# Kernel optimization log

Hardware: AMD Instinct MI355X
Metric: run time of the kernel (lower is better)

Reference implementation:

```python
import jax, jax.numpy as jnp
import numpy as np
from jax import lax

B, N, F_IN, F_OUT = 64, 256, 768, 256


def setup_inputs() -> dict:
    key = jax.random.key(0)
    ks = jax.random.split(key, 14)
    s = 0.02
    h = jax.random.normal(ks[0], (B, N, F_IN), jnp.float32)
    adj = jax.random.randint(ks[1], (B, N, N), 0, 2).astype(jnp.float32)
    return {
        'h': h,
        'adj': adj,
        'emb_W': jax.random.normal(ks[2], (F_OUT, F_IN), jnp.float32) * s,
        'ioux_W': jax.random.normal(ks[3], (2 * F_OUT, F_OUT), jnp.float32) * s,
        'ioux_b': jax.random.normal(ks[4], (2 * F_OUT,), jnp.float32) * s,
        'iouh_W': jax.random.normal(ks[5], (2 * F_OUT, F_OUT), jnp.float32) * s,
        'iouh_b': jax.random.normal(ks[6], (2 * F_OUT,), jnp.float32) * s,
        'coux_W': jax.random.normal(ks[7], (F_OUT, F_OUT), jnp.float32) * s,
        'coux_b': jax.random.normal(ks[8], (F_OUT,), jnp.float32) * s,
        'couh_W': jax.random.normal(ks[9], (F_OUT, F_OUT), jnp.float32) * s,
        'couh_b': jax.random.normal(ks[10], (F_OUT,), jnp.float32) * s,
        'fc_W': jax.random.normal(ks[11], (2, F_OUT), jnp.float32) * s,
        'fc_b': jax.random.normal(ks[12], (2,), jnp.float32) * s,
    }


def reference(h, adj, emb_W, ioux_W, ioux_b, iouh_W, iouh_b,
              coux_W, coux_b, couh_W, couh_b, fc_W, fc_b):
    # h: [B,N,F_IN], adj: [B,N,N]
    h_e = jnp.einsum('bnf,of->bno', h, emb_W)            # emb(h), no bias
    d = jnp.sum(adj, axis=-1)                            # row-degree [B,N]
    d_inv = jnp.where(d != 0, 1.0 / jnp.where(d != 0, d, 1.0), 0.0)
    # x-side projections depend only on the original h_e -> precompute once
    iou_x = jnp.einsum('bnf,of->bno', h_e, ioux_W) + ioux_b   # [B,N,2F]
    cou_x = jnp.einsum('bnf,of->bno', h_e, coux_W) + coux_b   # [B,N,F]

    n_nodes = h.shape[1]

    def step(h_copy, i):
        # Tree_Parent_AGG row i: p[b,i] = d_inv[b,i] * sum_j adj[b,j,i] * h_copy[b,j]
        adj_col = lax.dynamic_index_in_dim(adj, i, axis=2, keepdims=False)   # [B,N]
        dinv_i = lax.dynamic_index_in_dim(d_inv, i, axis=1, keepdims=False)  # [B]
        x_parent = jnp.einsum('bn,bnd->bd', adj_col, h_copy) * dinv_i[:, None]
        iou = lax.dynamic_index_in_dim(iou_x, i, axis=1, keepdims=False) \
              + x_parent @ iouh_W.T + iouh_b
        r, z = jnp.split(iou, 2, axis=1)
        r = jax.nn.sigmoid(r)
        z = jax.nn.sigmoid(z)
        hc = jnp.tanh(lax.dynamic_index_in_dim(cou_x, i, axis=1, keepdims=False)
                      + (r * x_parent) @ couh_W.T + couh_b)
        h_new = z * x_parent + (1.0 - z) * hc
        h_copy = lax.dynamic_update_index_in_dim(h_copy, h_new, i, axis=1)
        return h_copy, None

    h_final, _ = lax.scan(step, h_e, jnp.arange(n_nodes))
    pooled = jnp.max(h_final, axis=1)                    # [B,F]
    return pooled @ fc_W.T + fc_b                        # [B,2]
```

## Files before the change

kernel.cpp:

```cpp
#include <hip/hip_runtime.h>
#include <hip/hip_fp16.h>

#define NB    64
#define NN    256
#define FIN   768
#define FOUT  256

typedef _Float16 half8v __attribute__((ext_vector_type(8)));
typedef float    float4v __attribute__((ext_vector_type(4)));

__device__ inline unsigned char enc8(float v){
#if __has_builtin(__builtin_amdgcn_cvt_pk_fp8_f32)
  return (unsigned char)(__builtin_amdgcn_cvt_pk_fp8_f32(v, v, 0, false) & 0xFF);
#else
  float best = 1e30f; unsigned char bc = 0;
  for (int c = 0; c < 256; c++){
    if ((c & 0x7F) == 0x7F) continue;
    int e = (c >> 3) & 15, mnt = c & 7;
    float mag = e ? ldexpf(1.f + mnt*0.125f, e-7) : ldexpf(mnt*0.125f, -6);
    float d = (c >> 7) ? -mag : mag;
    float err = fabsf(v - d);
    if (err < best){ best = err; bc = (unsigned char)c; }
  }
  return bc;
#endif
}

__device__ inline float4v mfma_fp8(long long a, long long b, float4v c){
  return __builtin_amdgcn_mfma_f32_16x16x32_fp8_fp8(a, b, c, 0, 0, 0);
}
__device__ inline float4v mfma_f16(half8v a, half8v b, float4v c){
  return __builtin_amdgcn_mfma_f32_16x16x32_f16(a, b, c, 0, 0, 0);
}

__global__ __launch_bounds__(256) void setup_kernel(
    const float* __restrict__ emb_W, const float* __restrict__ ioux_W,
    const float* __restrict__ ioux_b, const float* __restrict__ coux_W,
    const float* __restrict__ coux_b,
    const float* __restrict__ iouh_W, const float* __restrict__ couh_W,
    const float* __restrict__ adj,
    _Float16* __restrict__ embW16, _Float16* __restrict__ Wcat16,
    float* __restrict__ biascat,
    unsigned char* __restrict__ iouh8, unsigned char* __restrict__ couh8,
    float* __restrict__ invrs_iou, float* __restrict__ invrs_cou,
    unsigned int* __restrict__ maskw, float* __restrict__ dinv)
{
  __shared__ float sm[256];
  __shared__ unsigned int rb[256][8];
  const int bid = blockIdx.x;
  const int t   = threadIdx.x;

  if (bid < 1539){
    int idx = bid*256 + t;
    if (idx < 196608) { embW16[idx] = (_Float16)emb_W[idx]; return; }
    idx -= 196608;
    if (idx < 196608) {
      int o = idx >> 8, k = idx & 255;
      float v = (o < 512) ? ioux_W[o*256 + k] : coux_W[(o-512)*256 + k];
      Wcat16[idx] = (_Float16)v; return;
    }
    idx -= 196608;
    if (idx < 768) biascat[idx] = (idx < 512) ? ioux_b[idx] : coux_b[idx-512];
    return;
  }

  if (bid < 2307){
    const int row = bid - 1539;
    const bool is_iou = (row < 512);
    const int rl = is_iou ? row : row - 512;
    const float w = is_iou ? iouh_W[(size_t)rl*256 + t] : couh_W[(size_t)rl*256 + t];
    sm[t] = fabsf(w);
    __syncthreads();
    for (int s = 128; s > 0; s >>= 1){
      if (t < s) sm[t] = fmaxf(sm[t], sm[t+s]);
      __syncthreads();
    }
    const float mx = sm[0];
    const float rs = (mx > 1e-20f) ? (240.0f / mx) : 1.0f;
    const unsigned char byte = enc8(w * rs);
    const int off = ((rl>>4)*8 + (t>>5))*512 + ((t>>3)&3)*128 + (rl&15)*8 + (t&7);
    if (is_iou) iouh8[off] = byte; else couh8[off] = byte;
    if (t == 0){
      const float inv = 1.0f / (rs * 16.0f);
      if (is_iou) invrs_iou[rl] = inv; else invrs_cou[rl] = inv;
    }
    return;
  }

  {
    const int b = bid - 2307;
    const float* rowp = adj + (size_t)b*NN*NN + (size_t)t*NN;
    float s = 0.f;
    #pragma unroll
    for (int qc = 0; qc < 8; qc++){
      unsigned int w = 0;
      const float4* rp = (const float4*)(rowp + qc*32);
      #pragma unroll
      for (int j4 = 0; j4 < 8; j4++){
        float4 v = rp[j4];
        s += v.x + v.y + v.z + v.w;
        const int sh = j4*4;
        w |= (v.x != 0.f ? 1u : 0u) << sh;
        w |= (v.y != 0.f ? 1u : 0u) << (sh+1);
        w |= (v.z != 0.f ? 1u : 0u) << (sh+2);
        w |= (v.w != 0.f ? 1u : 0u) << (sh+3);
      }
      rb[t][qc] = w;
    }
    dinv[b*NN + t] = (s != 0.f) ? 1.0f/s : 0.0f;
    __syncthreads();
    #pragma unroll
    for (int qc = 0; qc < 8; qc++){
      unsigned int w = 0;
      #pragma unroll
      for (int jj = 0; jj < 32; jj++)
        w |= ((rb[qc*32 + jj][t>>5] >> (t&31)) & 1u) << jj;
      maskw[((size_t)b*NN + t)*8 + qc] = w;
    }
  }
}

template<int AF32, int NTL>
__global__ __launch_bounds__(256) void gemm16_kernel(
    const void* __restrict__ Aq, const _Float16* __restrict__ Bw,
    _Float16* __restrict__ Cout, const float* __restrict__ bias,
    int M, int N, int K, int ldc)
{
  const int wave = threadIdx.x >> 6;
  const int lane = threadIdx.x & 63;
  const int m0 = (blockIdx.x*4 + wave)*16;
  const int n0 = blockIdx.y*(16*NTL);
  const int mrow = m0 + (lane & 15);
  const int kgrp = lane >> 4;
  float4v acc[NTL];
  #pragma unroll
  for (int nt = 0; nt < NTL; nt++) acc[nt] = (float4v){0.f,0.f,0.f,0.f};

  for (int k0 = 0; k0 < K; k0 += 32){
    const int ka = k0 + kgrp*8;
    half8v af;
    if (AF32){
      const float* A = (const float*)Aq;
      const float4* ap = (const float4*)(A + (size_t)mrow*K + ka);
      float4 a0 = ap[0], a1 = ap[1];
      af[0]=(_Float16)a0.x; af[1]=(_Float16)a0.y; af[2]=(_Float16)a0.z; af[3]=(_Float16)a0.w;
      af[4]=(_Float16)a1.x; af[5]=(_Float16)a1.y; af[6]=(_Float16)a1.z; af[7]=(_Float16)a1.w;
    } else {
      const _Float16* A = (const _Float16*)Aq;
      af = *(const half8v*)(A + (size_t)mrow*K + ka);
    }
    #pragma unroll
    for (int nt = 0; nt < NTL; nt++){
      const int ncol = n0 + nt*16 + (lane & 15);
      half8v bf = *(const half8v*)(Bw + (size_t)ncol*K + ka);
      acc[nt] = __builtin_amdgcn_mfma_f32_16x16x32_f16(af, bf, acc[nt], 0, 0, 0);
    }
  }
  #pragma unroll
  for (int nt = 0; nt < NTL; nt++){
    const int ncol = n0 + nt*16 + (lane & 15);
    const float bv = bias ? bias[ncol] : 0.f;
    #pragma unroll
    for (int r = 0; r < 4; r++){
      const int orow = m0 + (lane>>4)*4 + r;
      Cout[(size_t)orow*ldc + ncol] = (_Float16)(acc[nt][r] + bv);
    }
  }
}

__global__ __launch_bounds__(256) void tail_kernel(
    const _Float16* __restrict__ Hc, const _Float16* __restrict__ Wcat16,
    const float* __restrict__ biascat,
    _Float16* __restrict__ OUTX, _Float16* __restrict__ HcT)
{
  __shared__ _Float16 tile[32][264];
  const int bid = blockIdx.x;
  const int t   = threadIdx.x;

  if (bid < 1536){
    const int bx = bid & 255, seg = bid >> 8;
    const int wave = t >> 6;
    const int lane = t & 63;
    const int m0 = (bx*4 + wave)*16;
    const int n0 = seg*128;
    const int mrow = m0 + (lane & 15);
    const int kgrp = lane >> 4;
    float4v acc[8];
    #pragma unroll
    for (int nt = 0; nt < 8; nt++) acc[nt] = (float4v){0.f,0.f,0.f,0.f};
    for (int k0 = 0; k0 < 256; k0 += 32){
      const int ka = k0 + kgrp*8;
      const half8v af = *(const half8v*)(Hc + (size_t)mrow*256 + ka);
      #pragma unroll
      for (int nt = 0; nt < 8; nt++){
        const int ncol = n0 + nt*16 + (lane & 15);
        half8v bf = *(const half8v*)(Wcat16 + (size_t)ncol*256 + ka);
        acc[nt] = __builtin_amdgcn_mfma_f32_16x16x32_f16(af, bf, acc[nt], 0, 0, 0);
      }
    }
    #pragma unroll
    for (int nt = 0; nt < 8; nt++){
      const int ncol = n0 + nt*16 + (lane & 15);
      const float bv = biascat[ncol];
      #pragma unroll
      for (int r = 0; r < 4; r++){
        const int orow = m0 + (lane>>4)*4 + r;
        OUTX[(size_t)orow*768 + ncol] = (_Float16)(acc[nt][r] + bv);
      }
    }
    return;
  }

  {
    const int idx = bid - 1536;
    const int b = idx & 63, fg = idx >> 6;
    #pragma unroll
    for (int pass = 0; pass < 4; pass++){
      const int n  = pass*64 + (t>>2);
      const int f8 = (t&3)*8;
      const half8v v = *(const half8v*)(Hc + (size_t)(b*NN + n)*FOUT + fg*32 + f8);
      #pragma unroll
      for (int e = 0; e < 8; e++) tile[f8+e][n] = v[e];
    }
    __syncthreads();
    const int f = t>>3, ch = t&7;
    _Float16* dst = HcT + ((size_t)b*FOUT + fg*32 + f)*NN + ch*32;
    #pragma unroll
    for (int k = 0; k < 4; k++)
      *(half8v*)(dst + k*8) = *(const half8v*)(&tile[f][ch*32 + k*8]);
  }
}

#define OFF_BT   0
#define OFF_DT   33280
#define OFF_HNT  53760
#define OFF_XP32 74240
#define OFF_XP8  75264
#define OFF_P8   75520
#define OFF_Z    75776
#define OFF_PM   76800
#define OFF_MASK 77824
#define OFF_DINV 86016
#define SCAN_LDS 87040

__global__ __launch_bounds__(512, 2)
void scan_kernel(
    const _Float16* __restrict__ Hc,
    const _Float16* __restrict__ HcT,
    const _Float16* __restrict__ OUTX,
    const unsigned char* __restrict__ iouh8,
    const unsigned char* __restrict__ couh8,
    const float* __restrict__ invrs_iou,
    const float* __restrict__ invrs_cou,
    const float* __restrict__ dinv,
    const unsigned int* __restrict__ maskw,
    const float* __restrict__ iouh_b,
    const float* __restrict__ couh_b,
    const float* __restrict__ fc_W,
    const float* __restrict__ fc_b,
    float* __restrict__ out)
{
  const int b    = blockIdx.x;
  const int t    = threadIdx.x;
  const int wave = t >> 6;
  const int lane = t & 63;
  const int q    = lane >> 4;
  const int r    = lane & 15;
  const int f0   = 32*wave;

  extern __shared__ __align__(16) char smem[];
  float*         sh_xp32 = (float*)(smem + OFF_XP32);
  unsigned char* sh_xp8  = (unsigned char*)(smem + OFF_XP8);
  unsigned char* sh_p8   = (unsigned char*)(smem + OFF_P8);
  float*         sh_z    = (float*)(smem + OFF_Z);
  float*         sh_pm   = (float*)(smem + OFF_PM);
  unsigned int*  sh_mask = (unsigned int*)(smem + OFF_MASK);
  float*         sh_dinv = (float*)(smem + OFF_DINV);

  #pragma unroll
  for (int k = 0; k < 10; k++)
    ((unsigned int*)(smem + OFF_DT))[k*512 + t] = 0u;
  {
    const unsigned int* mg = maskw + ((size_t)b*NN)*8;
    #pragma unroll
    for (int k = 0; k < 4; k++) sh_mask[k*512 + t] = mg[k*512 + t];
    if (t < 256) sh_dinv[t] = dinv[(size_t)b*NN + t];
  }

  half8v Hreg[2][8];
  #pragma unroll
  for (int g = 0; g < 2; g++){
    const _Float16* hp = HcT + ((size_t)b*FOUT + f0 + 16*g + r)*NN + q*8;
    #pragma unroll
    for (int ks = 0; ks < 8; ks++)
      Hreg[g][ks] = *(const half8v*)(hp + ks*32);
  }

  long long ifrag[4][8];
  #pragma unroll
  for (int tt = 0; tt < 4; tt++)
    #pragma unroll
    for (int kc = 0; kc < 8; kc++)
      ifrag[tt][kc] = *(const long long*)(iouh8 + (size_t)(((4*wave+tt)*8 + kc)*512) + q*128 + r*8);
  long long cfrag[2][8];
  #pragma unroll
  for (int tt = 0; tt < 2; tt++)
    #pragma unroll
    for (int kc = 0; kc < 8; kc++)
      cfrag[tt][kc] = *(const long long*)(couh8 + (size_t)(((2*wave+tt)*8 + kc)*512) + q*128 + r*8);

  const int o1    = 64*wave + 16*(r>>2) + q*4 + (r&3);
  const int o_upd = 32*wave + 16*((r>>2)&1) + q*4 + (r&3);
  const float bi1 = iouh_b[o1];
  const float vi1 = invrs_iou[o1];
  const float bcou_l = couh_b[o_upd];
  const float invc_l = invrs_cou[o_upd];
  float pmax = -1e30f;

  __syncthreads();
  unsigned int wl_cur = sh_mask[0];

  #pragma unroll 1
  for (int i = 0; i < NN; i++){
    const size_t row = (size_t)b*NN + i;

    if ((i & 31) == 0){
      const int tile = i >> 5;
      if (tile > 0){
        const int tprev = tile - 1;
        #pragma unroll
        for (int g = 0; g < 2; g++){
          const half8v hv = *(const half8v*)(smem + OFF_HNT + (f0 + 16*g + r)*80 + q*16);
          #pragma unroll
          for (int ks = 0; ks < 8; ks++) if (ks == tprev) Hreg[g][ks] = hv;
        }
      }
      float4v bacc[2][2];
      #pragma unroll
      for (int rt = 0; rt < 2; rt++)
        #pragma unroll
        for (int g = 0; g < 2; g++) bacc[rt][g] = (float4v){0.f,0.f,0.f,0.f};
      #pragma unroll
      for (int rt = 0; rt < 2; rt++){
        #pragma unroll
        for (int ks = 0; ks < 8; ks++){
          const unsigned int wm = sh_mask[(i + rt*16 + r)*8 + ks];
          half8v am;
          #pragma unroll
          for (int e = 0; e < 8; e++)
            am[e] = (_Float16)((wm >> (q*8 + e)) & 1u);
          bacc[rt][0] = mfma_f16(am, Hreg[0][ks], bacc[rt][0]);
          bacc[rt][1] = mfma_f16(am, Hreg[1][ks], bacc[rt][1]);
        }
      }
      #pragma unroll
      for (int rt = 0; rt < 2; rt++)
        #pragma unroll
        for (int g = 0; g < 2; g++)
          #pragma unroll
          for (int jj = 0; jj < 4; jj++)
            *(float*)(smem + (rt*16 + q*4 + jj)*1040 + (f0 + 16*g + r)*4) = bacc[rt][g][jj];
    }

    const int li = i & 31;
    const unsigned int wl_next = sh_mask[((i+1)&255)*8 + (((i+1)>>5)&7)];
    const float oxi = (float)OUTX[row*768 + o1];
    const float oxc = (float)OUTX[row*768 + 512 + o_upd];
    const float he  = (float)Hc[row*FOUT + o_upd];
    const float dv  = sh_dinv[i];

    {
      const unsigned int wl = wl_cur & ((1u << li) - 1u);
      half8v af;
      #pragma unroll
      for (int e = 0; e < 8; e++)
        af[e] = (_Float16)((wl >> (q*8 + e)) & 1u);
      #pragma unroll
      for (int g = 0; g < 2; g++){
        const int fg = f0 + 16*g + r;
        const half8v bf = *(const half8v*)(smem + OFF_DT + fg*80 + q*16);
        float4v ag = (float4v){0.f,0.f,0.f,0.f};
        ag = mfma_f16(af, bf, ag);
        const float bt = *(const float*)(smem + li*1040 + fg*4);
        const float xp = (bt + ag[0]) * dv;
        if (q == 0)      sh_xp32[fg] = xp;
        else if (q == 1) sh_xp8[fg] = enc8(xp * 16.f);
      }
    }
    wl_cur = wl_next;
    __syncthreads();

    {
      float4v iacc[4];
      #pragma unroll
      for (int tt = 0; tt < 4; tt++) iacc[tt] = (float4v){0.f,0.f,0.f,0.f};
      #pragma unroll
      for (int kc = 0; kc < 8; kc++){
        const long long bfr = *(const long long*)(sh_xp8 + kc*32 + q*8);
        #pragma unroll
        for (int tt = 0; tt < 4; tt++)
          iacc[tt] = mfma_fp8(ifrag[tt][kc], bfr, iacc[tt]);
      }
      float d1 = 0.f;
      #pragma unroll
      for (int tt = 0; tt < 4; tt++) if ((r>>2) == tt){
        #pragma unroll
        for (int jj = 0; jj < 4; jj++) if ((r&3) == jj) d1 = iacc[tt][jj];
      }
      const float g1 = d1*vi1 + oxi + bi1;
      const float sg = 1.f / (1.f + __expf(-g1));
      if (wave < 4) sh_p8[o1] = enc8(sg * sh_xp32[o1] * 16.f);
      else          sh_z[o1 - 256] = sg;
    }
    __syncthreads();

    {
      float4v cacc[2];
      cacc[0] = (float4v){0.f,0.f,0.f,0.f};
      cacc[1] = cacc[0];
      #pragma unroll
      for (int kc = 0; kc < 8; kc++){
        const long long bfr = *(const long long*)(sh_p8 + kc*32 + q*8);
        cacc[0] = mfma_fp8(cfrag[0][kc], bfr, cacc[0]);
        cacc[1] = mfma_fp8(cfrag[1][kc], bfr, cacc[1]);
      }
      if (r < 8){
        float cd = 0.f;
        #pragma unroll
        for (int tt = 0; tt < 2; tt++) if ((r>>2) == tt){
          #pragma unroll
          for (int jj = 0; jj < 4; jj++) if ((r&3) == jj) cd = cacc[tt][jj];
        }
        const float v   = cd*invc_l + oxc + bcou_l;
        const float hcv = tanhf(v);
        const float z   = sh_z[o_upd];
        const float xpv = sh_xp32[o_upd];
        const float hn  = z*xpv + (1.f - z)*hcv;
        pmax = fmaxf(pmax, hn);
        *(_Float16*)(smem + OFF_DT  + o_upd*80 + li*2) = (_Float16)(hn - he);
        *(_Float16*)(smem + OFF_HNT + o_upd*80 + li*2) = (_Float16)hn;
      }
    }
  }

  if (r < 8) sh_pm[o_upd] = pmax;
  __syncthreads();
  if (t < 128){
    const int c = t >> 6;
    float s = 0.f;
    #pragma unroll
    for (int qq = 0; qq < 4; qq++){
      const int f = (t & 63) + qq*64;
      s += fc_W[c*256 + f] * sh_pm[f];
    }
    #pragma unroll
    for (int off = 32; off > 0; off >>= 1) s += __shfl_xor(s, off, 64);
    if ((t & 63) == 0) out[b*2 + c] = s + fc_b[c];
  }
}

extern "C" void kernel_launch(void* const* d_in, const int* in_sizes, int n_in,
                              void* d_out, int out_size, void* d_ws, size_t ws_size,
                              hipStream_t stream)
{
  (void)in_sizes; (void)n_in; (void)out_size; (void)ws_size;
  const float* h      = (const float*)d_in[0];
  const float* adj    = (const float*)d_in[1];
  const float* emb_W  = (const float*)d_in[2];
  const float* ioux_W = (const float*)d_in[3];
  const float* ioux_b = (const float*)d_in[4];
  const float* iouh_W = (const float*)d_in[5];
  const float* iouh_b = (const float*)d_in[6];
  const float* coux_W = (const float*)d_in[7];
  const float* coux_b = (const float*)d_in[8];
  const float* couh_W = (const float*)d_in[9];
  const float* couh_b = (const float*)d_in[10];
  const float* fc_W   = (const float*)d_in[11];
  const float* fc_b   = (const float*)d_in[12];
  float* out = (float*)d_out;

  size_t off = 0;
  char* base = (char*)d_ws;
  auto carve = [&](size_t bytes)->char* {
    off = (off + 255) & ~(size_t)255;
    char* p = base + off;
    off += bytes;
    return p;
  };
  _Float16* embW16 = (_Float16*)carve((size_t)256*768*2);
  _Float16* Wcat16 = (_Float16*)carve((size_t)768*256*2);
  float*    biascat= (float*)  carve((size_t)768*4);
  unsigned char* iouh8 = (unsigned char*)carve(131072);
  unsigned char* couh8 = (unsigned char*)carve(65536);
  float*    invrs_iou = (float*)carve(512*4);
  float*    invrs_cou = (float*)carve(256*4);
  float*    dinv   = (float*)  carve((size_t)NB*NN*4);
  unsigned int* maskw = (unsigned int*)carve((size_t)NB*NN*8*4 + 64);
  _Float16* Hc     = (_Float16*)carve((size_t)NB*NN*FOUT*2);
  _Float16* HcT    = (_Float16*)carve((size_t)NB*NN*FOUT*2);
  _Float16* OUTX   = (_Float16*)carve((size_t)NB*NN*768*2);

  hipFuncSetAttribute((const void*)scan_kernel,
                      hipFuncAttributeMaxDynamicSharedMemorySize, SCAN_LDS);

  setup_kernel<<<dim3(2371), dim3(256), 0, stream>>>(
      emb_W, ioux_W, ioux_b, coux_W, coux_b, iouh_W, couh_W, adj,
      embW16, Wcat16, biascat, iouh8, couh8, invrs_iou, invrs_cou,
      maskw, dinv);

  gemm16_kernel<1, 8><<<dim3(256, 2), dim3(256), 0, stream>>>(
      (const void*)h, embW16, Hc, nullptr, NB*NN, FOUT, FIN, FOUT);

  tail_kernel<<<dim3(2048), dim3(256), 0, stream>>>(
      Hc, Wcat16, biascat, OUTX, HcT);

  scan_kernel<<<dim3(NB), dim3(512), SCAN_LDS, stream>>>(
      Hc, HcT, OUTX, iouh8, couh8, invrs_iou, invrs_cou, dinv, maskw,
      iouh_b, couh_b, fc_W, fc_b, out);
}
```

Baseline: 616.2 us.

## Fuse embedding GEMM, x-projection GEMM and transpose into one kernel via LDS

Merges the embedding GEMM and the tail kernel (x-side projection GEMM plus Hc transpose) into a single mid_kernel. Each block computes a 64-row tile of Hc, keeps it in LDS, and reuses it for the projection GEMM and the transpose instead of re-reading Hc from global memory. This removes one launch and a global round trip. In exchange the grid shrinks to 256 blocks of 512 threads, which lowers parallelism for the projection GEMM. The diff calls an mfma_f16 helper that presumably lives in the part of the file not shown.

New measurement: 601.7 us. -2.4%, faster.

```diff
diff --git a/kernel.cpp b/kernel.cpp
--- a/kernel.cpp
+++ b/kernel.cpp
@@ -120,114 +120,102 @@
   }
 }
 
-template<int AF32, int NTL>
-__global__ __launch_bounds__(256) void gemm16_kernel(
-    const void* __restrict__ Aq, const _Float16* __restrict__ Bw,
-    _Float16* __restrict__ Cout, const float* __restrict__ bias,
-    int M, int N, int K, int ldc)
+__global__ __launch_bounds__(512) void mid_kernel(
+    const float* __restrict__ h, const _Float16* __restrict__ embW16,
+    const _Float16* __restrict__ Wcat16, const float* __restrict__ biascat,
+    _Float16* __restrict__ Hc, _Float16* __restrict__ OUTX,
+    _Float16* __restrict__ HcT)
 {
-  const int wave = threadIdx.x >> 6;
-  const int lane = threadIdx.x & 63;
-  const int m0 = (blockIdx.x*4 + wave)*16;
-  const int n0 = blockIdx.y*(16*NTL);
-  const int mrow = m0 + (lane & 15);
+  __shared__ _Float16 lds_hc[64][264];
+  const int bx   = blockIdx.x;
+  const int t    = threadIdx.x;
+  const int wave = t >> 6;
+  const int lane = t & 63;
+  const int rgrp = wave & 3;
+  const int cseg = wave >> 2;
+  const int m0g  = bx*64;
+  const int mrow = m0g + rgrp*16 + (lane & 15);
   const int kgrp = lane >> 4;
-  float4v acc[NTL];
-  #pragma unroll
-  for (int nt = 0; nt < NTL; nt++) acc[nt] = (float4v){0.f,0.f,0.f,0.f};
-
-  for (int k0 = 0; k0 < K; k0 += 32){
-    const int ka = k0 + kgrp*8;
-    half8v af;
-    if (AF32){
-      const float* A = (const float*)Aq;
-      const float4* ap = (const float4*)(A + (size_t)mrow*K + ka);
+
+  {
+    float4v acc[8];
+    #pragma unroll
+    for (int nt = 0; nt < 8; nt++) acc[nt] = (float4v){0.f,0.f,0.f,0.f};
+    for (int k0 = 0; k0 < FIN; k0 += 32){
+      const int ka = k0 + kgrp*8;
+      const float4* ap = (const float4*)(h + (size_t)mrow*FIN + ka);
       float4 a0 = ap[0], a1 = ap[1];
+      half8v af;
       af[0]=(_Float16)a0.x; af[1]=(_Float16)a0.y; af[2]=(_Float16)a0.z; af[3]=(_Float16)a0.w;
       af[4]=(_Float16)a1.x; af[5]=(_Float16)a1.y; af[6]=(_Float16)a1.z; af[7]=(_Float16)a1.w;
-    } else {
-      const _Float16* A = (const _Float16*)Aq;
-      af = *(const half8v*)(A + (size_t)mrow*K + ka);
-    }
-    #pragma unroll
-    for (int nt = 0; nt < NTL; nt++){
-      const int ncol = n0 + nt*16 + (lane & 15);
-      half8v bf = *(const half8v*)(Bw + (size_t)ncol*K + ka);
-      acc[nt] = __builtin_amdgcn_mfma_f32_16x16x32_f16(af, bf, acc[nt], 0, 0, 0);
-    }
-  }
-  #pragma unroll
-  for (int nt = 0; nt < NTL; nt++){
-    const int ncol = n0 + nt*16 + (lane & 15);
-    const float bv = bias ? bias[ncol] : 0.f;
-    #pragma unroll
-    for (int r = 0; r < 4; r++){
-      const int orow = m0 + (lane>>4)*4 + r;
-      Cout[(size_t)orow*ldc + ncol] = (_Float16)(acc[nt][r] + bv);
-    }
-  }
-}
-
-__global__ __launch_bounds__(256) void tail_kernel(
-    const _Float16* __restrict__ Hc, const _Float16* __restrict__ Wcat16,
-    const float* __restrict__ biascat,
-    _Float16* __restrict__ OUTX, _Float16* __restrict__ HcT)
-{
-  __shared__ _Float16 tile[32][264];
-  const int bid = blockIdx.x;
-  const int t   = threadIdx.x;
-
-  if (bid < 1536){
-    const int bx = bid & 255, seg = bid >> 8;
-    const int wave = t >> 6;
-    const int lane = t & 63;
-    const int m0 = (bx*4 + wave)*16;
-    const int n0 = seg*128;
-    const int mrow = m0 + (lane & 15);
-    const int kgrp = lane >> 4;
-    float4v acc[8];
-    #pragma unroll
-    for (int nt = 0; nt < 8; nt++) acc[nt] = (float4v){0.f,0.f,0.f,0.f};
-    for (int k0 = 0; k0 < 256; k0 += 32){
-      const int ka = k0 + kgrp*8;
-      const half8v af = *(const half8v*)(Hc + (size_t)mrow*256 + ka);
       #pragma unroll
       for (int nt = 0; nt < 8; nt++){
-        const int ncol = n0 + nt*16 + (lane & 15);
-        half8v bf = *(const half8v*)(Wcat16 + (size_t)ncol*256 + ka);
-        acc[nt] = __builtin_amdgcn_mfma_f32_16x16x32_f16(af, bf, acc[nt], 0, 0, 0);
+        const int ncol = cseg*128 + nt*16 + (lane & 15);
+        const half8v bf = *(const half8v*)(embW16 + (size_t)ncol*FIN + ka);
+        acc[nt] = mfma_f16(af, bf, acc[nt]);
       }
     }
     #pragma unroll
     for (int nt = 0; nt < 8; nt++){
-      const int ncol = n0 + nt*16 + (lane & 15);
-      const float bv = biascat[ncol];
-      #pragma unroll
-      for (int r = 0; r < 4; r++){
-        const int orow = m0 + (lane>>4)*4 + r;
-        OUTX[(size_t)orow*768 + ncol] = (_Float16)(acc[nt][r] + bv);
-      }
-    }
-    return;
-  }
+      const int ncol = cseg*128 + nt*16 + (lane & 15);
+      #pragma unroll
+      for (int r4 = 0; r4 < 4; r4++){
+        const int ol = rgrp*16 + (lane>>4)*4 + r4;
+        const _Float16 v = (_Float16)acc[nt][r4];
+        lds_hc[ol][ncol] = v;
+        Hc[(size_t)(m0g + ol)*FOUT + ncol] = v;
+      }
+    }
+  }
+  __syncthreads();
 
   {
-    const int idx = bid - 1536;
-    const int b = idx & 63, fg = idx >> 6;
-    #pragma unroll
-    for (int pass = 0; pass < 4; pass++){
-      const int n  = pass*64 + (t>>2);
-      const int f8 = (t&3)*8;
-      const half8v v = *(const half8v*)(Hc + (size_t)(b*NN + n)*FOUT + fg*32 + f8);
-      #pragma unroll
-      for (int e = 0; e < 8; e++) tile[f8+e][n] = v[e];
-    }
-    __syncthreads();
-    const int f = t>>3, ch = t&7;
-    _Float16* dst = HcT + ((size_t)b*FOUT + fg*32 + f)*NN + ch*32;
+    const int lrow = rgrp*16 + (lane & 15);
+    #pragma unroll
+    for (int pass = 0; pass < 3; pass++){
+      const int oc0 = cseg*384 + pass*128;
+      float4v acc[8];
+      #pragma unroll
+      for (int nt = 0; nt < 8; nt++) acc[nt] = (float4v){0.f,0.f,0.f,0.f};
+      for (int k0 = 0; k0 < FOUT; k0 += 32){
+        const int ka = k0 + kgrp*8;
+        const half8v af = *(const half8v*)(&lds_hc[lrow][ka]);
+        #pragma unroll
+        for (int nt = 0; nt < 8; nt++){
+          const int ncol = oc0 + nt*16 + (lane & 15);
+          const half8v bf = *(const half8v*)(Wcat16 + (size_t)ncol*FOUT + ka);
+          acc[nt] = mfma_f16(af, bf, acc[nt]);
+        }
+      }
+      #pragma unroll
+      for (int nt = 0; nt < 8; nt++){
+        const int ncol = oc0 + nt*16 + (lane & 15);
+        const float bv = biascat[ncol];
+        #pragma unroll
+        for (int r4 = 0; r4 < 4; r4++){
+          const int orow = m0g + rgrp*16 + (lane>>4)*4 + r4;
+          OUTX[(size_t)orow*768 + ncol] = (_Float16)(acc[nt][r4] + bv);
+        }
+      }
+    }
+  }
+
+  {
+    const int b  = bx >> 2;
+    const int n0 = (bx & 3)*64;
+    const int f  = t >> 1;
+    const int ch = t & 1;
+    unsigned short buf[32];
+    #pragma unroll
+    for (int j = 0; j < 32; j++){
+      union { _Float16 hv; unsigned short u; } cv;
+      cv.hv = lds_hc[ch*32 + j][f];
+      buf[j] = cv.u;
+    }
+    _Float16* dst = HcT + ((size_t)b*FOUT + f)*NN + n0 + ch*32;
     #pragma unroll
     for (int k = 0; k < 4; k++)
-      *(half8v*)(dst + k*8) = *(const half8v*)(&tile[f][ch*32 + k*8]);
+      *(uint4*)((char*)dst + k*16) = *(const uint4*)(&buf[k*8]);
   }
 }
 
@@ -508,11 +496,8 @@
       embW16, Wcat16, biascat, iouh8, couh8, invrs_iou, invrs_cou,
       maskw, dinv);
 
-  gemm16_kernel<1, 8><<<dim3(256, 2), dim3(256), 0, stream>>>(
-      (const void*)h, embW16, Hc, nullptr, NB*NN, FOUT, FIN, FOUT);
-
-  tail_kernel<<<dim3(2048), dim3(256), 0, stream>>>(
-      Hc, Wcat16, biascat, OUTX, HcT);
+  mid_kernel<<<dim3(256), dim3(512), 0, stream>>>(
+      h, embW16, Wcat16, biascat, Hc, OUTX, HcT);
 
   scan_kernel<<<dim3(NB), dim3(512), SCAN_LDS, stream>>>(
       Hc, HcT, OUTX, iouh8, couh8, invrs_iou, invrs_cou, dinv, maskw,
```
